# Performance work log

Hardware: AMD Instinct MI355X
Metric: run time of the kernel (lower is better)

Reference implementation:

```python
import jax, jax.numpy as jnp
import numpy as np

N = 100000      # total nodes (100 graphs x 1000 nodes each)
G = 100         # graphs per batch
F_IN = 12       # node_features (temporal window)
F_OUT = 32      # DCRNN hidden size (hardcoded in module)
K = 5           # diffusion (Chebyshev) steps (hardcoded)
C = 4           # num_classes
E = 16 * N      # edges: ring (N) + random (15N)


def setup_inputs() -> dict:
    key = jax.random.key(0)
    ks = jax.random.split(key, 12)
    x = jax.random.normal(ks[0], (N, F_IN), dtype=jnp.float32)
    ring = jnp.arange(N, dtype=jnp.int32)
    src = jnp.concatenate([ring, jax.random.randint(ks[1], (15 * N,), 0, N, dtype=jnp.int32)])
    dst = jnp.concatenate([(ring + 1) % N, jax.random.randint(ks[2], (15 * N,), 0, N, dtype=jnp.int32)])
    edge_index = jnp.stack([src, dst])  # [2, E]
    edge_weight = jax.random.uniform(ks[3], (E,), dtype=jnp.float32, minval=0.1, maxval=1.0)
    batch = (jnp.arange(N, dtype=jnp.int32) * G) // N  # sorted graph ids, 1000 nodes per graph
    s = 0.1
    return dict(
        x=x, edge_index=edge_index, edge_weight=edge_weight, batch=batch,
        W_z=jax.random.normal(ks[4], (2, K, F_IN + F_OUT, F_OUT), jnp.float32) * s,
        b_z=jax.random.normal(ks[5], (F_OUT,), jnp.float32) * s,
        W_r=jax.random.normal(ks[6], (2, K, F_IN + F_OUT, F_OUT), jnp.float32) * s,
        b_r=jax.random.normal(ks[7], (F_OUT,), jnp.float32) * s,
        W_h=jax.random.normal(ks[8], (2, K, F_IN + F_OUT, F_OUT), jnp.float32) * s,
        b_h=jax.random.normal(ks[9], (F_OUT,), jnp.float32) * s,
        W_lin=jax.random.normal(ks[10], (F_OUT, C), jnp.float32) * s,
        b_lin=jax.random.normal(ks[11], (C,), jnp.float32) * s,
    )


def reference(x, edge_index, edge_weight, batch, W_z, b_z, W_r, b_r, W_h, b_h, W_lin, b_lin):
    row, col = edge_index[0], edge_index[1]
    # weighted in/out degrees (to_dense_adj sums duplicate edges, same as segment_sum)
    deg_out_inv = 1.0 / jax.ops.segment_sum(edge_weight, row, num_segments=N)
    deg_in_inv = 1.0 / jax.ops.segment_sum(edge_weight, col, num_segments=N)
    norm_out = deg_out_inv[row][:, None]  # per-edge 1/deg_out(src)
    norm_in = deg_in_inv[row][:, None]    # per-edge 1/deg_in(src), as in DConv

    def prop_fwd(h):  # out[dst] += h[src]/deg_out[src]
        return jax.ops.segment_sum(norm_out * h[row], col, num_segments=N)

    def prop_rev(h):  # reverse (transposed) diffusion: out[src] += h[dst]/deg_in[src]
        return jax.ops.segment_sum(norm_in * h[col], row, num_segments=N)

    def dconv(Xc, W, b):
        # Chebyshev diffusion conv, W: [2, K, F_in+F_out, F_out]
        H = Xc @ (W[0, 0] + W[1, 0])
        T1o, T1i = prop_fwd(Xc), prop_rev(Xc)
        H = H + T1o @ W[0, 1] + T1i @ W[1, 1]
        T0o = T0i = Xc
        for k in range(2, K):
            T2o = 2.0 * prop_fwd(T1o) - T0o
            T2i = 2.0 * prop_rev(T1i) - T0i
            H = H + T2o @ W[0, k] + T2i @ W[1, k]
            T0o, T1o = T1o, T2o
            T0i, T1i = T1i, T2i
        return H + b

    # GRU gating with zero-initialized hidden state (H=None in module)
    Hst = jnp.zeros((N, F_OUT), x.dtype)
    XH = jnp.concatenate([x, Hst], axis=1)
    Z = jax.nn.sigmoid(dconv(XH, W_z, b_z))
    R = jax.nn.sigmoid(dconv(XH, W_r, b_r))
    XRH = jnp.concatenate([x, R * Hst], axis=1)
    H_tilde = jnp.tanh(dconv(XRH, W_h, b_h))
    H = Z * Hst + (1.0 - Z) * H_tilde

    h = jax.nn.relu(H) @ W_lin + b_lin            # [N, C]
    sums = jax.ops.segment_sum(h, batch, num_segments=G)
    counts = jax.ops.segment_sum(jnp.ones((N,), h.dtype), batch, num_segments=G)
    return sums / counts[:, None]                 # global_mean_pool -> [G, C]
```

## Files before the change

### kernel.cpp

```cpp
#include <hip/hip_runtime.h>
#include <math.h>

#define NN    100000
#define GG    100
#define FIN   12
#define FOUT  32
#define KD    5
#define CC    4
#define EE    1600000
#define ROWS  108
#define NBF   782
#define NBINS 1564
#define NBC   1024
#define CHUNK 1563
#define NSEG  (NBINS * NBC)

__device__ __forceinline__ int chunk_of_block(int b) {
    return ((b & 7) << 7) | (b >> 3);
}


__global__ __launch_bounds__(256) void k_hist(const int* __restrict__ ei,
                                              int* __restrict__ hist_g) {
    __shared__ int hist[NBINS];
    for (int i = threadIdx.x; i < NBINS; i += 256) hist[i] = 0;
    __syncthreads();
    int chunk = chunk_of_block(blockIdx.x);
    int lo = chunk * CHUNK, hi = lo + CHUNK;
    if (hi > EE) hi = EE;
    for (int e = lo + threadIdx.x; e < hi; e += 256) {
        int s = ei[e], d = ei[EE + e];
        atomicAdd(&hist[d >> 7], 1);
        atomicAdd(&hist[NBF + (s >> 7)], 1);
    }
    __syncthreads();
    for (int i = threadIdx.x; i < NBINS; i += 256)
        hist_g[i * NBC + blockIdx.x == 0 ? i * NBC + chunk : i * NBC + chunk] = hist[i];
}

__global__ __launch_bounds__(1024) void k_scan1(int* __restrict__ g,
                                                int* __restrict__ bsum) {
    __shared__ int sh[1024];
    int t = threadIdx.x;
    int i = blockIdx.x * 1024 + t;
    int v = g[i];
    sh[t] = v;
    __syncthreads();
    for (int d = 1; d < 1024; d <<= 1) {
        int x = sh[t];
        if (t >= d) x += sh[t - d];
        __syncthreads();
        sh[t] = x;
        __syncthreads();
    }
    g[i] = sh[t] - v;
    if (t == 1023) bsum[blockIdx.x] = sh[1023];
}

__global__ __launch_bounds__(1024) void k_scan2(int* __restrict__ bsum, int nb) {
    __shared__ int sh[1024];
    int t = threadIdx.x;
    int a = (2 * t     < nb) ? bsum[2 * t]     : 0;
    int b = (2 * t + 1 < nb) ? bsum[2 * t + 1] : 0;
    int s = a + b;
    sh[t] = s;
    __syncthreads();
    for (int d = 1; d < 1024; d <<= 1) {
        int x = sh[t];
        if (t >= d) x += sh[t - d];
        __syncthreads();
        sh[t] = x;
        __syncthreads();
    }
    int base = sh[t] - s;
    if (2 * t < nb)     bsum[2 * t] = base;
    if (2 * t + 1 < nb) bsum[2 * t + 1] = base + a;
}

__global__ __launch_bounds__(1024) void k_scan3(int* __restrict__ g,
                                                const int* __restrict__ bsum,
                                                int* __restrict__ off,
                                                int* __restrict__ off_node) {
    int i = blockIdx.x * 1024 + threadIdx.x;
    int v = g[i] + bsum[blockIdx.x];
    g[i] = v;
    if ((i & (NBC - 1)) == 0) off[i / NBC] = v;
    if (i == 0) { off[NBINS] = 2 * EE; off_node[2 * NN] = 2 * EE; }
}

__global__ __launch_bounds__(256) void k_place(const int* __restrict__ ei,
                                               const float* __restrict__ ew,
                                               const int* __restrict__ base_g,
                                               int2* __restrict__ recA) {
    __shared__ int cur[NBINS];
    int chunk = chunk_of_block(blockIdx.x);
    for (int i = threadIdx.x; i < NBINS; i += 256) cur[i] = base_g[i * NBC + chunk];
    __syncthreads();
    int lo = chunk * CHUNK, hi = lo + CHUNK;
    if (hi > EE) hi = EE;
    for (int e = lo + threadIdx.x; e < hi; e += 256) {
        int s = ei[e], d = ei[EE + e];
        float w = ew[e];
        int pf = atomicAdd(&cur[d >> 7], 1);
        recA[pf] = make_int2(s | ((d & 127) << 17), __float_as_int(w));
        int pr = atomicAdd(&cur[NBF + (s >> 7)], 1);
        recA[pr] = make_int2(d | ((s & 127) << 17), __float_as_int(w));
    }
}

__global__ __launch_bounds__(256) void k_subcsr(
        const int* __restrict__ off, const int2* __restrict__ recA,
        const float* __restrict__ x,
        int* __restrict__ off_node, int* __restrict__ rec2,
        float* __restrict__ dinv_in, float* __restrict__ dinv_out,
        float* __restrict__ gA) {
    __shared__ int   hist[128];
    __shared__ int   lofs[128];
    __shared__ int   cur[128];
    __shared__ float wsum[128];
    __shared__ float dl[128];
    int b = blockIdx.x;
    int t = threadIdx.x;
    if (t < 128) { hist[t] = 0; wsum[t] = 0.f; }
    __syncthreads();
    int e0 = off[b], e1 = off[b + 1];
    for (int e = e0 + t; e < e1; e += 256) {
        int2 r = recA[e];
        int loc = r.x >> 17;
        atomicAdd(&hist[loc], 1);
        atomicAdd(&wsum[loc], __int_as_float(r.y));
    }
    __syncthreads();
    if (t < 128) lofs[t] = hist[t];
    __syncthreads();
    for (int d = 1; d < 128; d <<= 1) {
        int v = 0;
        if (t < 128 && t >= d) v = lofs[t - d];
        __syncthreads();
        if (t < 128) lofs[t] += v;
        __syncthreads();
    }
    bool rev = b >= NBF;
    int base = (rev ? b - NBF : b) * 128;
    if (t < 128) {
        int ex = lofs[t] - hist[t];
        lofs[t] = ex;
        cur[t] = 0;
        int node = base + t;
        if (node < NN) {
            off_node[(rev ? NN : 0) + node] = e0 + ex;
            float inv = 1.f / wsum[t];
            dl[t] = inv;
            if (rev) dinv_out[node] = inv;
            else     dinv_in[node]  = inv;
        }
    }
    __syncthreads();
    for (int e = e0 + t; e < e1; e += 256) {
        int rx = recA[e].x;
        int loc = rx >> 17;
        int pos = e0 + lofs[loc] + atomicAdd(&cur[loc], 1);
        rec2[pos] = rx & 0x1FFFF;
    }
    if (rev) {
        __syncthreads();
        for (int i = t; i < 128 * 3; i += 256) {
            int loc = i / 3, ch = i - loc * 3;
            int node = base + loc;
            if (node < NN) {
                float4 v = *(const float4*)(x + (size_t)node * FIN + ch * 4);
                float sc = dl[loc];
                v.x *= sc; v.y *= sc; v.z *= sc; v.w *= sc;
                *(float4*)(gA + (size_t)node * FIN + ch * 4) = v;
            }
        }
    }
}


__global__ void k_misc(const float* __restrict__ Wz_in, const float* __restrict__ Wh_in,
                       float* __restrict__ Wz, float* __restrict__ Wh,
                       const float* __restrict__ b_lin, float* __restrict__ out) {
    int t = blockIdx.x * 256 + threadIdx.x;
    if (t < 2 * ROWS * FOUT) {
        int sel = t / (ROWS * FOUT);
        int rem = t - sel * ROWS * FOUT;
        int r = rem / FOUT;
        int f = rem - r * FOUT;
        int b = r / 12;
        int i = r - b * 12;
        const float* Ws = sel ? Wh_in : Wz_in;
        float v;
        if (b == 0)
            v = Ws[(0 * KD + 0) * 44 * 32 + i * 32 + f] + Ws[(1 * KD + 0) * 44 * 32 + i * 32 + f];
        else if (b <= 4)
            v = Ws[(0 * KD + b) * 44 * 32 + i * 32 + f];
        else
            v = Ws[(1 * KD + (b - 4)) * 44 * 32 + i * 32 + f];
        (sel ? Wh : Wz)[r * FOUT + f] = v;
    }
    int u = t - 2 * ROWS * FOUT;
    if (u >= 0 && u < GG * CC) out[u] = b_lin[u & 3];
}

#define LREC 2048
__global__ __launch_bounds__(256) void k_gather(
        const int* __restrict__ off_node, const int* __restrict__ rec2,
        const float* __restrict__ gIn, const float* __restrict__ hIn,
        const float* __restrict__ prevF, const float* __restrict__ prevR,
        const float* __restrict__ dinv_in, const float* __restrict__ dinv_out,
        float* __restrict__ outF, float* __restrict__ outR,
        float* __restrict__ gOut, float c) {
    __shared__ int lrec[LREC];
    int xcd = blockIdx.x & 7;
    int grp = blockIdx.x >> 3;
    bool rev = xcd >= 4;
    int dbase = rev ? NN : 0;
    int ub = (grp * 4 + (xcd & 3)) * 256;
    int lin = ub + threadIdx.x;

    int u1 = ub + 255; if (u1 > 3 * NN - 1) u1 = 3 * NN - 1;
    int node0 = ub / 3, node1 = u1 / 3;
    int w0 = off_node[dbase + node0];
    int w1 = off_node[dbase + node1 + 1];
    int wn = w1 - w0;
    bool useLds = (wn <= LREC);
    if (useLds) {
        for (int i = threadIdx.x; i < wn; i += 256) lrec[i] = rec2[w0 + i];
    }
    __syncthreads();

    if (lin < 3 * NN) {
        int node = lin / 3;
        int ch = lin - node * 3;
        int i0 = dbase + node;
        int e0 = off_node[i0], e1 = off_node[i0 + 1];
        const float* in = rev ? hIn : gIn;

        float ax = 0.f, ay = 0.f, az = 0.f, aw = 0.f;
        float bx = 0.f, by = 0.f, bz = 0.f, bw = 0.f;
        if (useLds) {
            int a0 = e0 - w0, a1 = e1 - w0;
            int e = a0;
            for (; e + 7 < a1; e += 8) {
                int n0 = lrec[e],     n1 = lrec[e + 1], n2 = lrec[e + 2], n3 = lrec[e + 3];
                int n4 = lrec[e + 4], n5 = lrec[e + 5], n6 = lrec[e + 6], n7 = lrec[e + 7];
                float4 v0 = *(const float4*)(in + (size_t)n0 * FIN + ch * 4);
                float4 v1 = *(const float4*)(in + (size_t)n1 * FIN + ch * 4);
                float4 v2 = *(const float4*)(in + (size_t)n2 * FIN + ch * 4);
                float4 v3 = *(const float4*)(in + (size_t)n3 * FIN + ch * 4);
                float4 v4 = *(const float4*)(in + (size_t)n4 * FIN + ch * 4);
                float4 v5 = *(const float4*)(in + (size_t)n5 * FIN + ch * 4);
                float4 v6 = *(const float4*)(in + (size_t)n6 * FIN + ch * 4);
                float4 v7 = *(const float4*)(in + (size_t)n7 * FIN + ch * 4);
                ax += v0.x; ay += v0.y; az += v0.z; aw += v0.w;
                bx += v1.x; by += v1.y; bz += v1.z; bw += v1.w;
                ax += v2.x; ay += v2.y; az += v2.z; aw += v2.w;
                bx += v3.x; by += v3.y; bz += v3.z; bw += v3.w;
                ax += v4.x; ay += v4.y; az += v4.z; aw += v4.w;
                bx += v5.x; by += v5.y; bz += v5.z; bw += v5.w;
                ax += v6.x; ay += v6.y; az += v6.z; aw += v6.w;
                bx += v7.x; by += v7.y; bz += v7.z; bw += v7.w;
            }
            for (; e < a1; ++e) {
                int n0 = lrec[e];
                float4 v0 = *(const float4*)(in + (size_t)n0 * FIN + ch * 4);
                ax += v0.x; ay += v0.y; az += v0.z; aw += v0.w;
            }
        } else {
            int e = e0;
            for (; e + 3 < e1; e += 4) {
                int n0 = rec2[e], n1 = rec2[e + 1], n2 = rec2[e + 2], n3 = rec2[e + 3];
                float4 v0 = *(const float4*)(in + (size_t)n0 * FIN + ch * 4);
                float4 v1 = *(const float4*)(in + (size_t)n1 * FIN + ch * 4);
                float4 v2 = *(const float4*)(in + (size_t)n2 * FIN + ch * 4);
                float4 v3 = *(const float4*)(in + (size_t)n3 * FIN + ch * 4);
                ax += v0.x; ay += v0.y; az += v0.z; aw += v0.w;
                bx += v1.x; by += v1.y; bz += v1.z; bw += v1.w;
                ax += v2.x; ay += v2.y; az += v2.z; aw += v2.w;
                bx += v3.x; by += v3.y; bz += v3.z; bw += v3.w;
            }
            for (; e < e1; ++e) {
                int n0 = rec2[e];
                float4 v0 = *(const float4*)(in + (size_t)n0 * FIN + ch * 4);
                ax += v0.x; ay += v0.y; az += v0.z; aw += v0.w;
            }
        }
        ax += bx; ay += by; az += bz; aw += bw;

        float sc = rev ? c * dinv_in[node] : c;
        ax *= sc; ay *= sc; az *= sc; aw *= sc;

        size_t o = (size_t)node * FIN + ch * 4;
        if (prevF) {
            float4 p = *(const float4*)((rev ? prevR : prevF) + o);
            ax -= p.x; ay -= p.y; az -= p.z; aw -= p.w;
        }
        float4 res = make_float4(ax, ay, az, aw);
        *(float4*)((rev ? outR : outF) + o) = res;
        if (!rev && gOut) {
            float g = dinv_out[node];
            res.x *= g; res.y *= g; res.z *= g; res.w *= g;
            *(float4*)(gOut + o) = res;
        }
    }
}


__global__ __launch_bounds__(256) void k_fused(
        const float* __restrict__ x, const float* __restrict__ TS,
        const float* __restrict__ Wz, const float* __restrict__ Wh,
        const float* __restrict__ bz, const float* __restrict__ bh,
        const float* __restrict__ Wlin, float* __restrict__ out) {
    __shared__ float rows[128][13];
    __shared__ float red[256 * CC];
    int g = blockIdx.x >> 3;
    int seg = blockIdx.x & 7;
    int base = g * 1000 + seg * 125;
    int tid = threadIdx.x;
    int lane = tid & 63;
    int wave = tid >> 6;
    int f0 = __builtin_amdgcn_readfirstlane(wave * 8);

    float az0[8], ah0[8], az1[8], ah1[8];
#pragma unroll
    for (int fi = 0; fi < 8; ++fi) {
        float vz = bz[f0 + fi], vh = bh[f0 + fi];
        az0[fi] = vz; ah0[fi] = vh; az1[fi] = vz; ah1[fi] = vh;
    }
    bool act1 = (lane + 64) < 125;

    for (int b = 0; b < 9; ++b) {
        const float* src = (b == 0) ? (x + (size_t)base * FIN)
                                    : (TS + ((size_t)(b - 1) * NN + base) * FIN);
        __syncthreads();
        for (int q = tid; q < 375; q += 256) {
            float4 v = *(const float4*)(src + q * 4);
            int e = q * 4;
            int n0 = e / 12,       i0 = e - n0 * 12;       rows[n0][i0] = v.x;
            int n1 = (e + 1) / 12, i1 = (e + 1) - n1 * 12; rows[n1][i1] = v.y;
            int n2 = (e + 2) / 12, i2 = (e + 2) - n2 * 12; rows[n2][i2] = v.z;
            int n3 = (e + 3) / 12, i3 = (e + 3) - n3 * 12; rows[n3][i3] = v.w;
        }
        __syncthreads();
        const float* wzr = Wz + b * 12 * FOUT + f0;
        const float* whr = Wh + b * 12 * FOUT + f0;
#pragma unroll
        for (int i = 0; i < FIN; ++i) {
            float v0 = rows[lane][i];
            float v1 = rows[lane + 64][i];
#pragma unroll
            for (int fi = 0; fi < 8; ++fi) {
                float wz = wzr[i * FOUT + fi];
                float wh = whr[i * FOUT + fi];
                az0[fi] = fmaf(v0, wz, az0[fi]);
                az1[fi] = fmaf(v1, wz, az1[fi]);
                ah0[fi] = fmaf(v0, wh, ah0[fi]);
                ah1[fi] = fmaf(v1, wh, ah1[fi]);
            }
        }
    }

    float o[CC] = {0.f, 0.f, 0.f, 0.f};
#pragma unroll
    for (int fi = 0; fi < 8; ++fi) {
        float z = 1.f / (1.f + __expf(-az0[fi]));
        float e2 = __expf(2.f * ah0[fi]);
        float th = 1.f - 2.f / (e2 + 1.f);
        float hv = fmaxf((1.f - z) * th, 0.f);
#pragma unroll
        for (int c = 0; c < CC; ++c) o[c] = fmaf(hv, Wlin[(f0 + fi) * 4 + c], o[c]);
    }
    if (act1) {
#pragma unroll
        for (int fi = 0; fi < 8; ++fi) {
            float z = 1.f / (1.f + __expf(-az1[fi]));
            float e2 = __expf(2.f * ah1[fi]);
            float th = 1.f - 2.f / (e2 + 1.f);
            float hv = fmaxf((1.f - z) * th, 0.f);
#pragma unroll
            for (int c = 0; c < CC; ++c) o[c] = fmaf(hv, Wlin[(f0 + fi) * 4 + c], o[c]);
        }
    }

#pragma unroll
    for (int c = 0; c < CC; ++c) red[tid * CC + c] = o[c];
    __syncthreads();
    for (int st = 128; st > 0; st >>= 1) {
        if (tid < st) {
#pragma unroll
            for (int c = 0; c < CC; ++c) red[tid * CC + c] += red[(tid + st) * CC + c];
        }
        __syncthreads();
    }
    if (tid == 0) {
#pragma unroll
        for (int c = 0; c < CC; ++c) atomicAdd(out + g * CC + c, red[c] * 0.001f);
    }
}


extern "C" void kernel_launch(void* const* d_in, const int* in_sizes, int n_in,
                              void* d_out, int out_size, void* d_ws, size_t ws_size,
                              hipStream_t stream) {
    const float* x     = (const float*)d_in[0];
    const int*   ei    = (const int*)d_in[1];
    const float* ew    = (const float*)d_in[2];
    const float* W_z   = (const float*)d_in[4];
    const float* b_z   = (const float*)d_in[5];
    const float* W_h   = (const float*)d_in[8];
    const float* b_h   = (const float*)d_in[9];
    const float* W_lin = (const float*)d_in[10];
    const float* b_lin = (const float*)d_in[11];
    float* out = (float*)d_out;

    int*   rec2     = (int*)d_ws;
    float* TS       = (float*)(rec2 + 2 * (size_t)EE);
    int2*  recA     = (int2*)TS;
    int*   hist_g   = rec2;
    int*   bsumS    = rec2 + NSEG;
    float* gA       = TS + (size_t)8 * NN * FIN;
    float* gB       = gA + (size_t)NN * FIN;
    float* dinv_in  = gB + (size_t)NN * FIN;
    float* dinv_out = dinv_in + NN;
    float* Wz       = dinv_out + NN;
    float* Wh       = Wz + ROWS * FOUT;
    int*   off      = (int*)(Wh + ROWS * FOUT);
    int*   off_node = off + NBINS + 1;

    float* T1o = TS + (size_t)0 * NN * FIN;
    float* T2o = TS + (size_t)1 * NN * FIN;
    float* T3o = TS + (size_t)2 * NN * FIN;
    float* T4o = TS + (size_t)3 * NN * FIN;
    float* T1i = TS + (size_t)4 * NN * FIN;
    float* T2i = TS + (size_t)5 * NN * FIN;
    float* T3i = TS + (size_t)6 * NN * FIN;
    float* T4i = TS + (size_t)7 * NN * FIN;

    dim3 B(256);
    int nbG = 2344;
    int nbScan = NSEG / 1024;

    k_hist<<<NBC, B, 0, stream>>>(ei, hist_g);
    k_scan1<<<nbScan, 1024, 0, stream>>>(hist_g, bsumS);
    k_scan2<<<1, 1024, 0, stream>>>(bsumS, nbScan);
    k_scan3<<<nbScan, 1024, 0, stream>>>(hist_g, bsumS, off, off_node);
    k_place<<<NBC, B, 0, stream>>>(ei, ew, hist_g, recA);
    k_subcsr<<<NBINS, B, 0, stream>>>(off, recA, x, off_node, rec2, dinv_in, dinv_out, gA);

    k_misc<<<(2 * ROWS * FOUT + GG * CC + 255) / 256, B, 0, stream>>>(W_z, W_h, Wz, Wh, b_lin, out);

    k_gather<<<nbG, B, 0, stream>>>(off_node, rec2, gA, x,   nullptr, nullptr, dinv_in, dinv_out, T1o, T1i, gB, 1.f);
    k_gather<<<nbG, B, 0, stream>>>(off_node, rec2, gB, T1i, x,       x,       dinv_in, dinv_out, T2o, T2i, gA, 2.f);
    k_gather<<<nbG, B, 0, stream>>>(off_node, rec2, gA, T2i, T1o,     T1i,     dinv_in, dinv_out, T3o, T3i, gB, 2.f);
    k_gather<<<nbG, B, 0, stream>>>(off_node, rec2, gB, T3i, T2o,     T2i,     dinv_in, dinv_out, T4o, T4i, nullptr, 2.f);

    k_fused<<<8 * GG, B, 0, stream>>>(x, TS, Wz, Wh, b_z, b_h, W_lin, out);
}
```

Baseline: 344.4 us.

## Store diffusion intermediates in bfloat16 to halve gather traffic

```diff
diff --git a/kernel.cpp b/kernel.cpp
--- a/kernel.cpp
+++ b/kernel.cpp
@@ -15,6 +15,16 @@
 #define CHUNK 1563
 #define NSEG  (NBINS * NBC)
 
+__device__ __forceinline__ unsigned bfr(float f) {
+    unsigned u = __float_as_uint(f);
+    return (u + 0x7FFFu + ((u >> 16) & 1u)) >> 16;
+}
+__device__ __forceinline__ unsigned pack2(float a, float b) {
+    return bfr(a) | (bfr(b) << 16);
+}
+#define BLO(u) __uint_as_float((u) << 16)
+#define BHI(u) __uint_as_float((u) & 0xFFFF0000u)
+
 __device__ __forceinline__ int chunk_of_block(int b) {
     return ((b & 7) << 7) | (b >> 3);
 }
@@ -35,7 +45,7 @@
     }
     __syncthreads();
     for (int i = threadIdx.x; i < NBINS; i += 256)
-        hist_g[i * NBC + blockIdx.x == 0 ? i * NBC + chunk : i * NBC + chunk] = hist[i];
+        hist_g[i * NBC + chunk] = hist[i];
 }
 
 __global__ __launch_bounds__(1024) void k_scan1(int* __restrict__ g,
@@ -113,7 +123,7 @@
         const float* __restrict__ x,
         int* __restrict__ off_node, int* __restrict__ rec2,
         float* __restrict__ dinv_in, float* __restrict__ dinv_out,
-        float* __restrict__ gA) {
+        uint2* __restrict__ gA) {
     __shared__ int   hist[128];
     __shared__ int   lofs[128];
     __shared__ int   cur[128];
@@ -165,13 +175,13 @@
     if (rev) {
         __syncthreads();
         for (int i = t; i < 128 * 3; i += 256) {
-            int loc = i / 3, ch = i - loc * 3;
+            int loc = i / 3, cc = i - loc * 3;
             int node = base + loc;
             if (node < NN) {
-                float4 v = *(const float4*)(x + (size_t)node * FIN + ch * 4);
+                float4 v = *(const float4*)(x + (size_t)node * FIN + cc * 4);
                 float sc = dl[loc];
-                v.x *= sc; v.y *= sc; v.z *= sc; v.w *= sc;
-                *(float4*)(gA + (size_t)node * FIN + ch * 4) = v;
+                gA[(size_t)node * 3 + cc] =
+                    make_uint2(pack2(v.x * sc, v.y * sc), pack2(v.z * sc, v.w * sc));
             }
         }
     }
@@ -180,7 +190,8 @@
 
 __global__ void k_misc(const float* __restrict__ Wz_in, const float* __restrict__ Wh_in,
                        float* __restrict__ Wz, float* __restrict__ Wh,
-                       const float* __restrict__ b_lin, float* __restrict__ out) {
+                       const float* __restrict__ b_lin, float* __restrict__ out,
+                       const float* __restrict__ x, uint2* __restrict__ xb) {
     int t = blockIdx.x * 256 + threadIdx.x;
     if (t < 2 * ROWS * FOUT) {
         int sel = t / (ROWS * FOUT);
@@ -201,16 +212,21 @@
     }
     int u = t - 2 * ROWS * FOUT;
     if (u >= 0 && u < GG * CC) out[u] = b_lin[u & 3];
+    if (t < 3 * NN) {
+        int n = t / 3, c = t - n * 3;
+        float4 v = *(const float4*)(x + (size_t)n * FIN + c * 4);
+        xb[(size_t)n * 3 + c] = make_uint2(pack2(v.x, v.y), pack2(v.z, v.w));
+    }
 }
 
 #define LREC 2048
 __global__ __launch_bounds__(256) void k_gather(
         const int* __restrict__ off_node, const int* __restrict__ rec2,
-        const float* __restrict__ gIn, const float* __restrict__ hIn,
-        const float* __restrict__ prevF, const float* __restrict__ prevR,
+        const uint2* __restrict__ gIn, const uint2* __restrict__ hIn,
+        const uint2* __restrict__ prevF, const uint2* __restrict__ prevR,
         const float* __restrict__ dinv_in, const float* __restrict__ dinv_out,
-        float* __restrict__ outF, float* __restrict__ outR,
-        float* __restrict__ gOut, float c) {
+        uint2* __restrict__ outF, uint2* __restrict__ outR,
+        uint2* __restrict__ gOut, float c) {
     __shared__ int lrec[LREC];
     int xcd = blockIdx.x & 7;
     int grp = blockIdx.x >> 3;
@@ -235,7 +251,7 @@
         int ch = lin - node * 3;
         int i0 = dbase + node;
         int e0 = off_node[i0], e1 = off_node[i0 + 1];
-        const float* in = rev ? hIn : gIn;
+        const uint2* in = rev ? hIn : gIn;
 
         float ax = 0.f, ay = 0.f, az = 0.f, aw = 0.f;
         float bx = 0.f, by = 0.f, bz = 0.f, bw = 0.f;
@@ -245,45 +261,33 @@
             for (; e + 7 < a1; e += 8) {
                 int n0 = lrec[e],     n1 = lrec[e + 1], n2 = lrec[e + 2], n3 = lrec[e + 3];
                 int n4 = lrec[e + 4], n5 = lrec[e + 5], n6 = lrec[e + 6], n7 = lrec[e + 7];
-                float4 v0 = *(const float4*)(in + (size_t)n0 * FIN + ch * 4);
-                float4 v1 = *(const float4*)(in + (size_t)n1 * FIN + ch * 4);
-                float4 v2 = *(const float4*)(in + (size_t)n2 * FIN + ch * 4);
-                float4 v3 = *(const float4*)(in + (size_t)n3 * FIN + ch * 4);
-                float4 v4 = *(const float4*)(in + (size_t)n4 * FIN + ch * 4);
-                float4 v5 = *(const float4*)(in + (size_t)n5 * FIN + ch * 4);
-                float4 v6 = *(const float4*)(in + (size_t)n6 * FIN + ch * 4);
-                float4 v7 = *(const float4*)(in + (size_t)n7 * FIN + ch * 4);
-                ax += v0.x; ay += v0.y; az += v0.z; aw += v0.w;
-                bx += v1.x; by += v1.y; bz += v1.z; bw += v1.w;
-                ax += v2.x; ay += v2.y; az += v2.z; aw += v2.w;
-                bx += v3.x; by += v3.y; bz += v3.z; bw += v3.w;
-                ax += v4.x; ay += v4.y; az += v4.z; aw += v4.w;
-                bx += v5.x; by += v5.y; bz += v5.z; bw += v5.w;
-                ax += v6.x; ay += v6.y; az += v6.z; aw += v6.w;
-                bx += v7.x; by += v7.y; bz += v7.z; bw += v7.w;
+                uint2 v0 = in[(size_t)n0 * 3 + ch];
+                uint2 v1 = in[(size_t)n1 * 3 + ch];
+                uint2 v2 = in[(size_t)n2 * 3 + ch];
+                uint2 v3 = in[(size_t)n3 * 3 + ch];
+                uint2 v4 = in[(size_t)n4 * 3 + ch];
+                uint2 v5 = in[(size_t)n5 * 3 + ch];
+                uint2 v6 = in[(size_t)n6 * 3 + ch];
+                uint2 v7 = in[(size_t)n7 * 3 + ch];
+                ax += BLO(v0.x); ay += BHI(v0.x); az += BLO(v0.y); aw += BHI(v0.y);
+                bx += BLO(v1.x); by += BHI(v1.x); bz += BLO(v1.y); bw += BHI(v1.y);
+                ax += BLO(v2.x); ay += BHI(v2.x); az += BLO(v2.y); aw += BHI(v2.y);
+                bx += BLO(v3.x); by += BHI(v3.x); bz += BLO(v3.y); bw += BHI(v3.y);
+                ax += BLO(v4.x); ay += BHI(v4.x); az += BLO(v4.y); aw += BHI(v4.y);
+                bx += BLO(v5.x); by += BHI(v5.x); bz += BLO(v5.y); bw += BHI(v5.y);
+                ax += BLO(v6.x); ay += BHI(v6.x); az += BLO(v6.y); aw += BHI(v6.y);
+                bx += BLO(v7.x); by += BHI(v7.x); bz += BLO(v7.y); bw += BHI(v7.y);
             }
             for (; e < a1; ++e) {
                 int n0 = lrec[e];
-                float4 v0 = *(const float4*)(in + (size_t)n0 * FIN + ch * 4);
-                ax += v0.x; ay += v0.y; az += v0.z; aw += v0.w;
+                uint2 v0 = in[(size_t)n0 * 3 + ch];
+                ax += BLO(v0.x); ay += BHI(v0.x); az += BLO(v0.y); aw += BHI(v0.y);
             }
         } else {
-            int e = e0;
-            for (; e + 3 < e1; e += 4) {
-                int n0 = rec2[e], n1 = rec2[e + 1], n2 = rec2[e + 2], n3 = rec2[e + 3];
-                float4 v0 = *(const float4*)(in + (size_t)n0 * FIN + ch * 4);
-                float4 v1 = *(const float4*)(in + (size_t)n1 * FIN + ch * 4);
-                float4 v2 = *(const float4*)(in + (size_t)n2 * FIN + ch * 4);
-                float4 v3 = *(const float4*)(in + (size_t)n3 * FIN + ch * 4);
-                ax += v0.x; ay += v0.y; az += v0.z; aw += v0.w;
-                bx += v1.x; by += v1.y; bz += v1.z; bw += v1.w;
-                ax += v2.x; ay += v2.y; az += v2.z; aw += v2.w;
-                bx += v3.x; by += v3.y; bz += v3.z; bw += v3.w;
-            }
-            for (; e < e1; ++e) {
+            for (int e = e0; e < e1; ++e) {
                 int n0 = rec2[e];
-                float4 v0 = *(const float4*)(in + (size_t)n0 * FIN + ch * 4);
-                ax += v0.x; ay += v0.y; az += v0.z; aw += v0.w;
+                uint2 v0 = in[(size_t)n0 * 3 + ch];
+                ax += BLO(v0.x); ay += BHI(v0.x); az += BLO(v0.y); aw += BHI(v0.y);
             }
         }
         ax += bx; ay += by; az += bz; aw += bw;
@@ -291,24 +295,22 @@
         float sc = rev ? c * dinv_in[node] : c;
         ax *= sc; ay *= sc; az *= sc; aw *= sc;
 
-        size_t o = (size_t)node * FIN + ch * 4;
+        size_t o = (size_t)node * 3 + ch;
         if (prevF) {
-            float4 p = *(const float4*)((rev ? prevR : prevF) + o);
-            ax -= p.x; ay -= p.y; az -= p.z; aw -= p.w;
-        }
-        float4 res = make_float4(ax, ay, az, aw);
-        *(float4*)((rev ? outR : outF) + o) = res;
+            uint2 p = (rev ? prevR : prevF)[o];
+            ax -= BLO(p.x); ay -= BHI(p.x); az -= BLO(p.y); aw -= BHI(p.y);
+        }
+        (rev ? outR : outF)[o] = make_uint2(pack2(ax, ay), pack2(az, aw));
         if (!rev && gOut) {
             float g = dinv_out[node];
-            res.x *= g; res.y *= g; res.z *= g; res.w *= g;
-            *(float4*)(gOut + o) = res;
+            gOut[o] = make_uint2(pack2(g * ax, g * ay), pack2(g * az, g * aw));
         }
     }
 }
 
 
 __global__ __launch_bounds__(256) void k_fused(
-        const float* __restrict__ x, const float* __restrict__ TS,
+        const float* __restrict__ x, const uint2* __restrict__ TS2,
         const float* __restrict__ Wz, const float* __restrict__ Wh,
         const float* __restrict__ bz, const float* __restrict__ bh,
         const float* __restrict__ Wlin, float* __restrict__ out) {
@@ -331,16 +333,27 @@
     bool act1 = (lane + 64) < 125;
 
     for (int b = 0; b < 9; ++b) {
-        const float* src = (b == 0) ? (x + (size_t)base * FIN)
-                                    : (TS + ((size_t)(b - 1) * NN + base) * FIN);
-        __syncthreads();
-        for (int q = tid; q < 375; q += 256) {
-            float4 v = *(const float4*)(src + q * 4);
-            int e = q * 4;
-            int n0 = e / 12,       i0 = e - n0 * 12;       rows[n0][i0] = v.x;
-            int n1 = (e + 1) / 12, i1 = (e + 1) - n1 * 12; rows[n1][i1] = v.y;
-            int n2 = (e + 2) / 12, i2 = (e + 2) - n2 * 12; rows[n2][i2] = v.z;
-            int n3 = (e + 3) / 12, i3 = (e + 3) - n3 * 12; rows[n3][i3] = v.w;
+        __syncthreads();
+        if (b == 0) {
+            const float* src = x + (size_t)base * FIN;
+            for (int q = tid; q < 375; q += 256) {
+                float4 v = *(const float4*)(src + q * 4);
+                int e = q * 4;
+                int n0 = e / 12,       i0 = e - n0 * 12;       rows[n0][i0] = v.x;
+                int n1 = (e + 1) / 12, i1 = (e + 1) - n1 * 12; rows[n1][i1] = v.y;
+                int n2 = (e + 2) / 12, i2 = (e + 2) - n2 * 12; rows[n2][i2] = v.z;
+                int n3 = (e + 3) / 12, i3 = (e + 3) - n3 * 12; rows[n3][i3] = v.w;
+            }
+        } else {
+            const uint2* Tb = TS2 + (size_t)(b - 1) * NN * 3;
+            for (int q = tid; q < 375; q += 256) {
+                int n = q / 3, cc = q - n * 3;
+                uint2 v = Tb[(size_t)(base + n) * 3 + cc];
+                rows[n][cc * 4 + 0] = BLO(v.x);
+                rows[n][cc * 4 + 1] = BHI(v.x);
+                rows[n][cc * 4 + 2] = BLO(v.y);
+                rows[n][cc * 4 + 3] = BHI(v.y);
+            }
         }
         __syncthreads();
         const float* wzr = Wz + b * 12 * FOUT + f0;
@@ -415,31 +428,37 @@
     float* out = (float*)d_out;
 
     int*   rec2     = (int*)d_ws;
-    float* TS       = (float*)(rec2 + 2 * (size_t)EE);
-    int2*  recA     = (int2*)TS;
+    unsigned* TSb   = (unsigned*)(rec2 + 2 * (size_t)EE);
+    int2*  recA     = (int2*)TSb;
     int*   hist_g   = rec2;
     int*   bsumS    = rec2 + NSEG;
-    float* gA       = TS + (size_t)8 * NN * FIN;
-    float* gB       = gA + (size_t)NN * FIN;
-    float* dinv_in  = gB + (size_t)NN * FIN;
+    unsigned* gAu   = TSb + (size_t)8 * NN * 6 + 1600000;
+    unsigned* gBu   = gAu + (size_t)NN * 6;
+    unsigned* xbu   = gBu + (size_t)NN * 6;
+    float* dinv_in  = (float*)(xbu + (size_t)NN * 6);
     float* dinv_out = dinv_in + NN;
     float* Wz       = dinv_out + NN;
     float* Wh       = Wz + ROWS * FOUT;
     int*   off      = (int*)(Wh + ROWS * FOUT);
     int*   off_node = off + NBINS + 1;
 
-    float* T1o = TS + (size_t)0 * NN * FIN;
-    float* T2o = TS + (size_t)1 * NN * FIN;
-    float* T3o = TS + (size_t)2 * NN * FIN;
-    float* T4o = TS + (size_t)3 * NN * FIN;
-    float* T1i = TS + (size_t)4 * NN * FIN;
-    float* T2i = TS + (size_t)5 * NN * FIN;
-    float* T3i = TS + (size_t)6 * NN * FIN;
-    float* T4i = TS + (size_t)7 * NN * FIN;
+    uint2* TS2 = (uint2*)TSb;
+    uint2* T1o = TS2 + (size_t)0 * NN * 3;
+    uint2* T2o = TS2 + (size_t)1 * NN * 3;
+    uint2* T3o = TS2 + (size_t)2 * NN * 3;
+    uint2* T4o = TS2 + (size_t)3 * NN * 3;
+    uint2* T1i = TS2 + (size_t)4 * NN * 3;
+    uint2* T2i = TS2 + (size_t)5 * NN * 3;
+    uint2* T3i = TS2 + (size_t)6 * NN * 3;
+    uint2* T4i = TS2 + (size_t)7 * NN * 3;
+    uint2* gA = (uint2*)gAu;
+    uint2* gB = (uint2*)gBu;
+    uint2* xb = (uint2*)xbu;
 
     dim3 B(256);
     int nbG = 2344;
     int nbScan = NSEG / 1024;
+    int nbMisc = (3 * NN + 255) / 256;
 
     k_hist<<<NBC, B, 0, stream>>>(ei, hist_g);
     k_scan1<<<nbScan, 1024, 0, stream>>>(hist_g, bsumS);
@@ -448,12 +467,12 @@
     k_place<<<NBC, B, 0, stream>>>(ei, ew, hist_g, recA);
     k_subcsr<<<NBINS, B, 0, stream>>>(off, recA, x, off_node, rec2, dinv_in, dinv_out, gA);
 
-    k_misc<<<(2 * ROWS * FOUT + GG * CC + 255) / 256, B, 0, stream>>>(W_z, W_h, Wz, Wh, b_lin, out);
-
-    k_gather<<<nbG, B, 0, stream>>>(off_node, rec2, gA, x,   nullptr, nullptr, dinv_in, dinv_out, T1o, T1i, gB, 1.f);
-    k_gather<<<nbG, B, 0, stream>>>(off_node, rec2, gB, T1i, x,       x,       dinv_in, dinv_out, T2o, T2i, gA, 2.f);
+    k_misc<<<nbMisc, B, 0, stream>>>(W_z, W_h, Wz, Wh, b_lin, out, x, xb);
+
+    k_gather<<<nbG, B, 0, stream>>>(off_node, rec2, gA, xb,  nullptr, nullptr, dinv_in, dinv_out, T1o, T1i, gB, 1.f);
+    k_gather<<<nbG, B, 0, stream>>>(off_node, rec2, gB, T1i, xb,      xb,      dinv_in, dinv_out, T2o, T2i, gA, 2.f);
     k_gather<<<nbG, B, 0, stream>>>(off_node, rec2, gA, T2i, T1o,     T1i,     dinv_in, dinv_out, T3o, T3i, gB, 2.f);
     k_gather<<<nbG, B, 0, stream>>>(off_node, rec2, gB, T3i, T2o,     T2i,     dinv_in, dinv_out, T4o, T4i, nullptr, 2.f);
 
-    k_fused<<<8 * GG, B, 0, stream>>>(x, TS, Wz, Wh, b_z, b_h, W_lin, out);
-}
+    k_fused<<<8 * GG, B, 0, stream>>>(x, TS2, Wz, Wh, b_z, b_h, W_lin, out);
+}
```

Result: faster. 310.5 us (median of 2 runs) (-9.9%).
